# Kernel tuning notes

Measured on AMD Instinct MI355X. Metric: run time of the kernel, lower is better.

Reference implementation:

```python
import jax, jax.numpy as jnp
import numpy as np

V, D, B, P = 50000, 128, 1024, 50
N, E = B * P, B * P
SCALE = 12.0


def _norm(x):
    return jnp.linalg.norm(x, axis=-1, keepdims=True)


def setup_inputs():
    key = jax.random.key(0)
    ks = jax.random.split(key, 32)
    stdv = 1.0 / np.sqrt(D)

    def u(k, shape):
        return jax.random.uniform(k, shape, minval=-stdv, maxval=stdv, dtype=jnp.float32)

    iid = jax.random.randint(ks[0], (N,), 0, V)
    # edges stay inside each session's node block [g*P, (g+1)*P)
    base = jnp.repeat(jnp.arange(B) * P, P)
    edge_src = base + jax.random.randint(ks[1], (E,), 0, P)
    edge_dst = base + jax.random.randint(ks[2], (E,), 0, P)
    node_gid = jnp.repeat(jnp.arange(B), P)          # session id per node
    last_nodes = jnp.arange(B) * P + (P - 1)          # nodes with data['last']==1
    edge_w = jax.random.uniform(ks[3], (E,), minval=0.1, maxval=1.0)
    edge_t = jax.random.uniform(ks[4], (E,))
    params = dict(
        embedding=u(ks[5], (V, D)),
        W1=u(ks[6], (D, 2 * D)), W2=u(ks[7], (D, 2 * D)),
        gru_wih=u(ks[8], (3 * D, 4 * D)), gru_whh=u(ks[9], (3 * D, D)),
        gru_bih=u(ks[10], (3 * D,)), gru_bhh=u(ks[11], (3 * D,)),
        Wxr=u(ks[12], (D, D)), bxr=u(ks[13], (D,)),
        Wxz=u(ks[14], (D, D)), bxz=u(ks[15], (D,)),
        Wxh=u(ks[16], (D, D)), bxh=u(ks[17], (D,)),
        Whr=u(ks[18], (D, D)), bhr=u(ks[19], (D,)),
        Whz=u(ks[20], (D, D)), bhz=u(ks[21], (D,)),
        Whh=u(ks[22], (D, D)), bhh=u(ks[23], (D,)),
        fc_u=u(ks[24], (D, D)),
        fc_vw=u(ks[25], (D, D)), fc_vb=u(ks[26], (D,)),
        fc_e=u(ks[27], (D,)),
        fc_sr=u(ks[28], (2 * D, D)),
    )
    return dict(iid=iid, edge_src=edge_src, edge_dst=edge_dst, node_gid=node_gid,
                last_nodes=last_nodes, edge_w=edge_w, edge_t=edge_t, **params)


def reference(iid, edge_src, edge_dst, node_gid, last_nodes, edge_w, edge_t,
              embedding, W1, W2, gru_wih, gru_whh, gru_bih, gru_bhh,
              Wxr, bxr, Wxz, bxz, Wxh, bxh, Whr, bhr, Whz, bhz, Whh, bhh,
              fc_u, fc_vw, fc_vb, fc_e, fc_sr):
    segN = lambda d, ids: jax.ops.segment_sum(d, ids, num_segments=N)
    feat = embedding[iid]
    feat = feat / (_norm(feat) + 1e-12)

    # --- GGNNLayer (num_layers=1): weighted-mean over in-edges and reversed graph ---
    ws_in = segN(edge_w, edge_dst)
    ws_out = segN(edge_w, edge_src)
    m_in = segN(feat[edge_src] * edge_w[:, None], edge_dst)
    m_out = segN(feat[edge_dst] * edge_w[:, None], edge_src)
    neigh1 = m_in / jnp.where(ws_in > 0, ws_in, 1.0)[:, None]   # zero-degree -> 0 (DGL default)
    neigh2 = m_out / jnp.where(ws_out > 0, ws_out, 1.0)[:, None]
    hn = jnp.concatenate([neigh1 @ W1, neigh2 @ W2], axis=1)    # [N, 4D]
    gi = hn @ gru_wih.T + gru_bih
    gh = feat @ gru_whh.T + gru_bhh
    ir, iz, inn = jnp.split(gi, 3, axis=1)
    hr, hz, hnn = jnp.split(gh, 3, axis=1)
    r = jax.nn.sigmoid(ir + hr)
    z = jax.nn.sigmoid(iz + hz)
    n = jnp.tanh(inn + r * hnn)
    feat = (1.0 - z) * n + z * feat                              # GRUCell update
    feat = feat / jnp.maximum(_norm(feat), 1e-12)                # F.normalize

    # --- GraphGRUODE: one RK4 step on [0, t_end]; per-eval time-filtered symmetric GCN ---
    x = feat
    no_self = edge_src != edge_dst

    def gcn(h, em, W, b):
        # DGL GraphConv norm='both' on the masked graph + its reverse edges
        deg = segN(em, edge_src) + segN(em, edge_dst)
        nrm = jnp.maximum(deg, 1.0) ** -0.5
        hs = h * nrm[:, None]
        me = em[:, None]
        agg = segN(hs[edge_src] * me, edge_dst) + segN(hs[edge_dst] * me, edge_src)
        return (agg * nrm[:, None]) @ W + b

    def f(tv, h):
        em = ((edge_t <= tv) & no_self).astype(h.dtype)
        xr = gcn(x, em, Wxr, bxr)
        xz = gcn(x, em, Wxz, bxz)
        xh = gcn(x, em, Wxh, bxh)
        r_ = jax.nn.sigmoid(xr + gcn(h, em, Whr, bhr))
        z_ = jax.nn.sigmoid(xz + gcn(h, em, Whz, bhz))
        u_ = jnp.tanh(xh + gcn(r_ * h, em, Whh, bhh))
        dh = (1.0 - z_) * (u_ - h)
        return dh / jnp.maximum(_norm(dh), 1e-12)                # F.normalize

    dt = edge_t.max()
    k1 = f(jnp.float32(0.0), feat)
    k2 = f(dt * 0.5, feat + dt * 0.5 * k1)
    k3 = f(dt * 0.5, feat + dt * 0.5 * k2)
    k4 = f(dt, feat + dt * k3)
    feat = feat + (dt / 6.0) * (k1 + 2.0 * k2 + 2.0 * k3 + k4)
    feat = feat / _norm(feat)                                    # torch code divides with no eps here

    # --- AttnReadout (batch_norm disabled, fc_out is None) ---
    fu = feat @ fc_u
    fv = feat[last_nodes] @ fc_vw + fc_vb                        # [B, D]
    e = jax.nn.sigmoid(fu + fv[node_gid]) @ fc_e                 # [N]
    emax = jax.ops.segment_max(e, node_gid, num_segments=B)
    ee = jnp.exp(e - emax[node_gid])
    alpha = ee / jax.ops.segment_sum(ee, node_gid, num_segments=B)[node_gid]
    sr_g = jax.ops.segment_sum(feat * alpha[:, None], node_gid, num_segments=B)
    sr = jnp.concatenate([feat[last_nodes], sr_g], axis=1) @ fc_sr
    sr = sr / (_norm(sr) + 1e-12)

    target = embedding / (_norm(embedding) + 1e-12)
    logits = sr @ target.T                                       # [B, V]
    return jax.nn.log_softmax(SCALE * logits, axis=-1)
```

## Files before the change

### kernel.cpp

```cpp
#include <hip/hip_runtime.h>
#include <math.h>

constexpr int V_ = 50000, D_ = 128, B_ = 1024, P_ = 50;
constexpr int N_ = 51200, E_ = 51200;
constexpr long long NS_ = (long long)N_ * D_;
constexpr float SCALE_ = 12.0f;
constexpr int NBN_L = (V_ + 127) / 128;
constexpr int NBN_P = 392;

typedef unsigned short u16;
typedef __attribute__((ext_vector_type(8))) unsigned short u16x8;
typedef __attribute__((ext_vector_type(8))) __bf16 bf16x8;
typedef __attribute__((ext_vector_type(4))) float f32x4;

static __device__ __forceinline__ float wsum(float v) {
    #pragma unroll
    for (int o = 32; o; o >>= 1) v += __shfl_xor(v, o, 64);
    return v;
}
static __device__ __forceinline__ float wmax(float v) {
    #pragma unroll
    for (int o = 32; o; o >>= 1) v = fmaxf(v, __shfl_xor(v, o, 64));
    return v;
}
static __device__ __forceinline__ float fsig(float x) { return 1.f / (1.f + __expf(-x)); }
static __device__ __forceinline__ float ftanh(float x) { return 2.f / (1.f + __expf(-2.f * x)) - 1.f; }
static __device__ __forceinline__ u16 f2b(float x) {
    unsigned u = __float_as_uint(x);
    u += 0x7fffu + ((u >> 16) & 1u);
    return (u16)(u >> 16);
}
static __device__ __forceinline__ float b2f(u16 u) {
    return __uint_as_float(((unsigned)u) << 16);
}
static __device__ __forceinline__ float redlr(float v) {
    v += __shfl_xor(v, 1, 64); v += __shfl_xor(v, 2, 64);
    v += __shfl_xor(v, 4, 64); v += __shfl_xor(v, 8, 64);
    return v;
}

__global__ void k_embcv(const float* __restrict__ emb, u16* __restrict__ embb,
                        float* __restrict__ rnv) {
    int row = blockIdx.x * 4 + (threadIdx.x >> 6);
    if (row >= V_) return;
    int l = threadIdx.x & 63;
    const float* p = emb + (long long)row * D_;
    float a = p[l], b = p[l + 64];
    float ss = wsum(a * a + b * b);
    if (l == 0) rnv[row] = 1.f / (sqrtf(ss) + 1e-12f);
    u16* q = embb + (long long)row * D_;
    q[l] = f2b(a); q[l + 64] = f2b(b);
}

__global__ void k_dtmax(const float* __restrict__ et, float* __restrict__ dt) {
    __shared__ float s[1024];
    float m = 0.f;
    for (int i = threadIdx.x; i < E_; i += 1024) m = fmaxf(m, et[i]);
    s[threadIdx.x] = m; __syncthreads();
    for (int o = 512; o; o >>= 1) {
        if (threadIdx.x < o) s[threadIdx.x] = fmaxf(s[threadIdx.x], s[threadIdx.x + o]);
        __syncthreads();
    }
    if (threadIdx.x == 0) *dt = s[0];
}

__global__ void k_feat0(const u16* __restrict__ embb, const float* __restrict__ rnv,
                        const int* __restrict__ iid, u16* __restrict__ featb) {
    int row = blockIdx.x * 4 + (threadIdx.x >> 6);
    int l = threadIdx.x & 63;
    int id = iid[row];
    const u16* p = embb + (long long)id * D_;
    float s = rnv[id];
    u16* qb = featb + (long long)row * D_;
    qb[l] = f2b(b2f(p[l]) * s); qb[l + 64] = f2b(b2f(p[l + 64]) * s);
}

__global__ void k_aggA_g(const int* __restrict__ esrc, const int* __restrict__ edst,
                         const float* __restrict__ ew, const u16* __restrict__ featb,
                         u16* __restrict__ m_in, u16* __restrict__ m_out) {
    __shared__ float sfeat[P_ * D_];
    __shared__ float smin[P_ * D_];
    __shared__ float smout[P_ * D_];
    __shared__ int ses[P_], sed[P_];
    __shared__ float sw[P_], swin[P_], swout[P_];
    int g = blockIdx.x, t = threadIdx.x;
    int n0 = g * P_;
    long long base = (long long)n0 * D_;
    for (int i = t; i < P_ * D_; i += 256) {
        sfeat[i] = b2f(featb[base + i]);
        smin[i] = 0.f; smout[i] = 0.f;
    }
    if (t < P_) {
        int E0 = g * P_ + t;
        ses[t] = esrc[E0] - n0;
        sed[t] = edst[E0] - n0;
        sw[t] = ew[E0];
    }
    __syncthreads();
    int d = t & 127;
    for (int e = 0; e < P_; e++) {
        int ls = ses[e], ld = sed[e];
        float w = sw[e];
        if (t < 128) smin[ld * D_ + d] += sfeat[ls * D_ + d] * w;
        else         smout[ls * D_ + d] += sfeat[ld * D_ + d] * w;
    }
    if (t < P_) {
        float wi = 0.f, wo = 0.f;
        for (int e = 0; e < P_; e++) {
            if (sed[e] == t) wi += sw[e];
            if (ses[e] == t) wo += sw[e];
        }
        swin[t] = (wi > 0.f) ? 1.f / wi : 1.f;
        swout[t] = (wo > 0.f) ? 1.f / wo : 1.f;
    }
    __syncthreads();
    for (int i = t; i < P_ * D_; i += 256) {
        int n = i >> 7;
        m_in[base + i] = f2b(smin[i] * swin[n]);
        m_out[base + i] = f2b(smout[i] * swout[n]);
    }
}

__global__ void k_prec_all(const float* __restrict__ W1, const float* __restrict__ W2,
                           const float* __restrict__ wih, const float* __restrict__ whh,
                           const float* __restrict__ bih, const float* __restrict__ bhh,
                           const float* __restrict__ Wxr, const float* __restrict__ Wxz,
                           const float* __restrict__ Whr, const float* __restrict__ Whz,
                           const float* __restrict__ bxr, const float* __restrict__ bxz,
                           const float* __restrict__ bhr, const float* __restrict__ bhz,
                           const float* __restrict__ Wxh, const float* __restrict__ Whh,
                           const float* __restrict__ bxh, const float* __restrict__ bhh2,
                           const float* __restrict__ fcu,
                           u16* __restrict__ BM1t, u16* __restrict__ BM2t, u16* __restrict__ BM3t,
                           u16* __restrict__ Brz1, u16* __restrict__ Brz2,
                           u16* __restrict__ Bu1, u16* __restrict__ Bu2, u16* __restrict__ Bfc,
                           float* __restrict__ b512, float* __restrict__ brz,
                           float* __restrict__ bu) {
    int blk = blockIdx.x, t = threadIdx.x;
    if (blk < 512) {
        const float* W = (blk < 256) ? W1 : W2;
        int coff = (blk < 256) ? 0 : 256;
        u16* Bt = (blk < 256) ? BM1t : BM2t;
        int idx = (blk & 255) * 256 + t;
        int j = idx >> 7, k = idx & 127;
        float s = 0.f;
        if (j < 384) {
            const float* wr = W + (long long)k * 256;
            const float* ir = wih + (long long)j * 512 + coff;
            for (int c = 0; c < 256; c++) s += wr[c] * ir[c];
        }
        Bt[idx] = f2b(s);
    } else if (blk < 768) {
        int idx = (blk - 512) * 256 + t;
        int j = idx >> 7, k = idx & 127;
        float v = 0.f;
        if (j < 256) v = whh[(long long)j * 128 + k];
        else if (j >= 384) v = whh[(long long)(j - 128) * 128 + k];
        BM3t[idx] = f2b(v);
    } else if (blk < 896) {
        int idx = (blk - 768) * 256 + t;
        int c = idx >> 7, k = idx & 127;
        float v1 = (c < 128) ? Wxr[(long long)k * 128 + c] : Wxz[(long long)k * 128 + (c - 128)];
        float v2 = (c < 128) ? Whr[(long long)k * 128 + c] : Whz[(long long)k * 128 + (c - 128)];
        Brz1[idx] = f2b(v1); Brz2[idx] = f2b(v2);
        if (k == 0) brz[c] = (c < 128) ? bxr[c] + bhr[c] : bxz[c - 128] + bhz[c - 128];
    } else if (blk < 960) {
        int idx = (blk - 896) * 256 + t;
        int c = idx >> 7, k = idx & 127;
        Bu1[idx] = f2b(Wxh[(long long)k * 128 + c]);
        Bu2[idx] = f2b(Whh[(long long)k * 128 + c]);
        if (k == 0) bu[c] = bxh[c] + bhh2[c];
    } else if (blk < 1024) {
        int idx = (blk - 960) * 256 + t;
        int c = idx >> 7, k = idx & 127;
        Bfc[idx] = f2b(fcu[(long long)k * 128 + c]);
    } else {
        int j = (blk - 1024) * 256 + t;
        if (j < 512) {
            float v;
            if (j < 256) v = bih[j] + bhh[j];
            else if (j < 384) v = bih[j];
            else v = bhh[j - 128];
            b512[j] = v;
        }
    }
}

template<int NSEG, int ACT>
__launch_bounds__(256)
__global__ void k_mm(const u16* __restrict__ A1, const u16* __restrict__ A2,
                     const u16* __restrict__ A3,
                     const u16* __restrict__ B1, const u16* __restrict__ B2,
                     const u16* __restrict__ B3,
                     const float* __restrict__ bias,
                     u16* __restrict__ C, int ldc, int nbn) {
    __shared__ u16 As[128 * 40];
    __shared__ u16 Bs[128 * 40];
    const int t = threadIdx.x;
    const int bid = blockIdx.x;
    const int xcd = bid & 7, idx = bid >> 3;
    const int nbm8 = gridDim.x / (8 * nbn);
    const int bm = xcd * nbm8 + idx / nbn;
    const int bn = idx % nbn;
    const int lane = t & 63, wid = t >> 6;
    const int wr = wid >> 1, wc = wid & 1;
    const int lr = lane & 15, lh = lane >> 4;
    f32x4 acc[4][4] = {};
    constexpr int KTOT = NSEG * 128;
    for (int ks = 0; ks < KTOT; ks += 32) {
        const u16* Ap = (NSEG == 1) ? A1 : (ks < 128 ? A1 : (ks < 256 ? A2 : A3));
        const u16* Bp = (NSEG == 1) ? B1 : (ks < 128 ? B1 : (ks < 256 ? B2 : B3));
        int kk = ks & 127;
        #pragma unroll
        for (int i = 0; i < 2; i++) {
            int id2 = i * 256 + t;
            int row = id2 >> 2, kl = (id2 & 3) * 8;
            u16x8 va = *(const u16x8*)&Ap[((long long)bm * 128 + row) * 128 + kk + kl];
            *(u16x8*)&As[row * 40 + kl] = va;
            u16x8 vb = *(const u16x8*)&Bp[((long long)bn * 128 + row) * 128 + kk + kl];
            *(u16x8*)&Bs[row * 40 + kl] = vb;
        }
        __syncthreads();
        bf16x8 af[4], bf[4];
        #pragma unroll
        for (int f = 0; f < 4; f++) {
            u16x8 ar = *(const u16x8*)&As[(wr * 64 + f * 16 + lr) * 40 + lh * 8];
            u16x8 br = *(const u16x8*)&Bs[(wc * 64 + f * 16 + lr) * 40 + lh * 8];
            af[f] = __builtin_bit_cast(bf16x8, ar);
            bf[f] = __builtin_bit_cast(bf16x8, br);
        }
        #pragma unroll
        for (int fr = 0; fr < 4; fr++)
            #pragma unroll
            for (int fc = 0; fc < 4; fc++)
                acc[fr][fc] = __builtin_amdgcn_mfma_f32_16x16x32_bf16(af[fr], bf[fc], acc[fr][fc], 0, 0, 0);
        __syncthreads();
    }
    #pragma unroll
    for (int fc = 0; fc < 4; fc++) {
        int col = bn * 128 + wc * 64 + fc * 16 + lr;
        float bb = bias ? bias[col] : 0.f;
        #pragma unroll
        for (int fr = 0; fr < 4; fr++) {
            int rowl = wr * 64 + fr * 16 + lh * 4;
            long long row0 = (long long)bm * 128 + rowl;
            #pragma unroll
            for (int r = 0; r < 4; r++) {
                float v = acc[fr][fc][r] + bb;
                if (ACT == 1) v = fsig(v);
                else if (ACT == 2) v = ftanh(v);
                C[(row0 + r) * (long long)ldc + col] = f2b(v);
            }
        }
    }
}

__global__ void k_gru2(const u16* __restrict__ gih, u16* __restrict__ featb,
                       u16* __restrict__ hb) {
    int row = blockIdx.x * 4 + (threadIdx.x >> 6);
    int l = threadIdx.x & 63;
    const u16* g = gih + (long long)row * 512;
    u16* fb = featb + (long long)row * 128;
    float nv[2]; float ss = 0.f;
    #pragma unroll
    for (int tq = 0; tq < 2; tq++) {
        int d = l + tq * 64;
        float r = fsig(b2f(g[d]));
        float z = fsig(b2f(g[128 + d]));
        float n = ftanh(b2f(g[256 + d]) + r * b2f(g[384 + d]));
        float fv = b2f(fb[d]);
        nv[tq] = (1.f - z) * n + z * fv;
        ss += nv[tq] * nv[tq];
    }
    ss = wsum(ss);
    float s = 1.f / fmaxf(sqrtf(ss), 1e-12f);
    u16 a = f2b(nv[0] * s), b = f2b(nv[1] * s);
    fb[l] = a; fb[l + 64] = b;
    u16* hh = hb + (long long)row * 128;
    hh[l] = a; hh[l + 64] = b;
}

template<int FIN>
__launch_bounds__(512, 8)
__global__ void k_fstep(const int* __restrict__ esrc, const int* __restrict__ edst,
                        const float* __restrict__ et, const float* __restrict__ dtp,
                        float tfac, int h_is_x, int axmode,
                        u16* __restrict__ featb, u16* __restrict__ hb,
                        u16* __restrict__ AXg, u16* __restrict__ RHG, u16* __restrict__ ZG,
                        u16* __restrict__ accg,
                        const u16* __restrict__ Brz1, const u16* __restrict__ Brz2,
                        const float* __restrict__ brz,
                        const u16* __restrict__ Bu1, const u16* __restrict__ Bu2,
                        const float* __restrict__ bu,
                        float accw, float hfac, int first) {
    constexpr int AS = 136;
    __shared__ u16 sAX[64 * AS];
    __shared__ u16 sAH[64 * AS];
    __shared__ float snrm[P_];
    __shared__ int ses[P_], sed[P_], sdeg[P_], soff[P_ + 1], snbr[2 * P_];
    __shared__ float ssqW[4][64];
    const int g = blockIdx.x, t = threadIdx.x;
    const int n0 = g * P_;
    const long long base = (long long)n0 * D_;
    const int wv = t >> 6, lane = t & 63;
    const int lr = lane & 15, lh = lane >> 4;
    const float dt = dtp[0];
    const float tv = tfac * dt;

    for (int i = t; i < 64 * AS; i += 512) { sAX[i] = 0; sAH[i] = 0; }
    if (t < P_) {
        int E0 = g * P_ + t;
        int ss_ = esrc[E0] - n0, dd = edst[E0] - n0;
        bool ml = (ss_ != dd) && (et[E0] <= tv);
        ses[t] = ml ? ss_ : -1;
        sed[t] = ml ? dd : -1;
    }
    __syncthreads();
    if (t < P_) {
        int dg = 0;
        for (int e = 0; e < P_; e++) dg += (ses[e] == t) + (sed[e] == t);
        sdeg[t] = dg;
        snrm[t] = rsqrtf(fmaxf((float)dg, 1.f));
    }
    __syncthreads();
    if (t < 64) {
        int v = (t < P_) ? sdeg[t] : 0;
        int inc = v;
        #pragma unroll
        for (int o = 1; o < 64; o <<= 1) {
            int u = __shfl_up(inc, o, 64);
            if (t >= o) inc += u;
        }
        if (t < P_) soff[t] = inc - v;
        if (t == P_ - 1) soff[P_] = inc;
    }
    __syncthreads();
    if (t < P_) {
        int c = soff[t];
        for (int e = 0; e < P_; e++) {
            if (ses[e] == t) snbr[c++] = sed[e];
            if (sed[e] == t) snbr[c++] = ses[e];
        }
    }
    __syncthreads();

    const int d = t & 127, grp = t >> 7;
    const int nlo = grp * 13, nhi = (grp * 13 + 13 < P_) ? grp * 13 + 13 : P_;
    if (axmode == 2) {
        for (int n = nlo; n < nhi; n++)
            sAX[n * AS + d] = AXg[base + (long long)n * D_ + d];
    } else {
        for (int n = nlo; n < nhi; n++) {
            float a = 0.f;
            for (int j = soff[n]; j < soff[n + 1]; j++) {
                int nb = snbr[j];
                a += b2f(featb[base + (long long)nb * D_ + d]) * snrm[nb];
            }
            u16 v = f2b(a * snrm[n]);
            sAX[n * AS + d] = v;
            if (axmode == 1) AXg[base + (long long)n * D_ + d] = v;
        }
    }
    if (!h_is_x) {
        for (int n = nlo; n < nhi; n++) {
            float a = 0.f;
            for (int j = soff[n]; j < soff[n + 1]; j++) {
                int nb = snbr[j];
                a += b2f(hb[base + (long long)nb * D_ + d]) * snrm[nb];
            }
            sAH[n * AS + d] = f2b(a * snrm[n]);
        }
    }
    __syncthreads();
    {
        const u16* A2 = h_is_x ? sAX : sAH;
        f32x4 acc[4][2] = {};
        for (int ks = 0; ks < 256; ks += 32) {
            const u16* Ap = (ks < 128) ? sAX : A2;
            const u16* Bp = (ks < 128) ? Brz1 : Brz2;
            int kk = ks & 127;
            bf16x8 af[4], bf[2];
            #pragma unroll
            for (int f = 0; f < 4; f++) {
                u16x8 ar = *(const u16x8*)&Ap[(f * 16 + lr) * AS + kk + lh * 8];
                af[f] = __builtin_bit_cast(bf16x8, ar);
            }
            #pragma unroll
            for (int f = 0; f < 2; f++) {
                int col = wv * 32 + f * 16 + lr;
                u16x8 br = *(const u16x8*)&Bp[(long long)col * 128 + kk + lh * 8];
                bf[f] = __builtin_bit_cast(bf16x8, br);
            }
            #pragma unroll
            for (int fr = 0; fr < 4; fr++)
                #pragma unroll
                for (int fc = 0; fc < 2; fc++)
                    acc[fr][fc] = __builtin_amdgcn_mfma_f32_16x16x32_bf16(af[fr], bf[fc], acc[fr][fc], 0, 0, 0);
        }
        #pragma unroll
        for (int fc = 0; fc < 2; fc++) {
            int col = wv * 32 + fc * 16 + lr;
            float bb = brz[col];
            #pragma unroll
            for (int fr = 0; fr < 4; fr++) {
                int row0 = fr * 16 + lh * 4;
                #pragma unroll
                for (int r = 0; r < 4; r++) {
                    int row = row0 + r;
                    if (row < P_) {
                        float v = fsig(acc[fr][fc][r] + bb);
                        long long ix = base + (long long)row * D_;
                        if (col < 128) RHG[ix + col] = f2b(v * b2f(hb[ix + col]));
                        else           ZG[ix + col - 128] = f2b(v);
                    }
                }
            }
        }
    }
    __syncthreads();
    for (int n = nlo; n < nhi; n++) {
        float a = 0.f;
        for (int j = soff[n]; j < soff[n + 1]; j++) {
            int nb = snbr[j];
            a += b2f(RHG[base + (long long)nb * D_ + d]) * snrm[nb];
        }
        sAH[n * AS + d] = f2b(a * snrm[n]);
    }
    __syncthreads();
    const int wr = wv >> 2, wc = wv & 3;
    f32x4 acc[2][2] = {};
    for (int ks = 0; ks < 256; ks += 32) {
        const u16* Ap = (ks < 128) ? sAX : sAH;
        const u16* Bp = (ks < 128) ? Bu1 : Bu2;
        int kk = ks & 127;
        bf16x8 af[2], bf[2];
        #pragma unroll
        for (int f = 0; f < 2; f++) {
            u16x8 ar = *(const u16x8*)&Ap[(wr * 32 + f * 16 + lr) * AS + kk + lh * 8];
            af[f] = __builtin_bit_cast(bf16x8, ar);
        }
        #pragma unroll
        for (int f = 0; f < 2; f++) {
            int col = wc * 32 + f * 16 + lr;
            u16x8 br = *(const u16x8*)&Bp[(long long)col * 128 + kk + lh * 8];
            bf[f] = __builtin_bit_cast(bf16x8, br);
        }
        #pragma unroll
        for (int fr = 0; fr < 2; fr++)
            #pragma unroll
            for (int fc = 0; fc < 2; fc++)
                acc[fr][fc] = __builtin_amdgcn_mfma_f32_16x16x32_bf16(af[fr], bf[fc], acc[fr][fc], 0, 0, 0);
    }
    float pr[2][4] = {};
    #pragma unroll
    for (int fc = 0; fc < 2; fc++) {
        int col = wc * 32 + fc * 16 + lr;
        float bb = bu[col];
        #pragma unroll
        for (int fr = 0; fr < 2; fr++) {
            int row0 = wr * 32 + fr * 16 + lh * 4;
            #pragma unroll
            for (int r = 0; r < 4; r++) {
                int row = row0 + r;
                float v = 0.f;
                if (row < P_) {
                    long long ix = base + (long long)row * D_ + col;
                    float u = ftanh(acc[fr][fc][r] + bb);
                    float z = b2f(ZG[ix]);
                    float hh = b2f(hb[ix]);
                    v = (1.f - z) * (u - hh);
                }
                acc[fr][fc][r] = v;
                pr[fr][r] += v * v;
            }
        }
    }
    #pragma unroll
    for (int fr = 0; fr < 2; fr++)
        #pragma unroll
        for (int r = 0; r < 4; r++) {
            float v = redlr(pr[fr][r]);
            if (lr == 0) ssqW[wc][wr * 32 + fr * 16 + lh * 4 + r] = v;
        }
    __syncthreads();
    if (FIN) {
        float dt6 = dt / 6.f;
        float pr2[2][4] = {};
        #pragma unroll
        for (int fr = 0; fr < 2; fr++) {
            int row0 = wr * 32 + fr * 16 + lh * 4;
            #pragma unroll
            for (int r = 0; r < 4; r++) {
                int row = row0 + r;
                float sc = 0.f;
                if (row < P_) {
                    float ssum = ssqW[0][row] + ssqW[1][row] + ssqW[2][row] + ssqW[3][row];
                    sc = 1.f / fmaxf(sqrtf(ssum), 1e-12f);
                }
                #pragma unroll
                for (int fc = 0; fc < 2; fc++) {
                    int col = wc * 32 + fc * 16 + lr;
                    float fv2 = 0.f;
                    if (row < P_) {
                        long long ix = base + (long long)row * D_ + col;
                        float kv = acc[fr][fc][r] * sc;
                        float an = b2f(accg[ix]) + accw * kv;
                        fv2 = b2f(featb[ix]) + dt6 * an;
                    }
                    acc[fr][fc][r] = fv2;
                    pr2[fr][r] += fv2 * fv2;
                }
            }
        }
        __syncthreads();
        #pragma unroll
        for (int fr = 0; fr < 2; fr++)
            #pragma unroll
            for (int r = 0; r < 4; r++) {
                float v = redlr(pr2[fr][r]);
                if (lr == 0) ssqW[wc][wr * 32 + fr * 16 + lh * 4 + r] = v;
            }
        __syncthreads();
        #pragma unroll
        for (int fr = 0; fr < 2; fr++) {
            int row0 = wr * 32 + fr * 16 + lh * 4;
            #pragma unroll
            for (int r = 0; r < 4; r++) {
                int row = row0 + r;
                if (row >= P_) continue;
                float ssum = ssqW[0][row] + ssqW[1][row] + ssqW[2][row] + ssqW[3][row];
                float s2 = 1.f / sqrtf(ssum);
                #pragma unroll
                for (int fc = 0; fc < 2; fc++) {
                    int col = wc * 32 + fc * 16 + lr;
                    featb[base + (long long)row * D_ + col] = f2b(acc[fr][fc][r] * s2);
                }
            }
        }
    } else {
        #pragma unroll
        for (int fr = 0; fr < 2; fr++) {
            int row0 = wr * 32 + fr * 16 + lh * 4;
            #pragma unroll
            for (int r = 0; r < 4; r++) {
                int row = row0 + r;
                if (row >= P_) continue;
                float ssum = ssqW[0][row] + ssqW[1][row] + ssqW[2][row] + ssqW[3][row];
                float sc = 1.f / fmaxf(sqrtf(ssum), 1e-12f);
                #pragma unroll
                for (int fc = 0; fc < 2; fc++) {
                    int col = wc * 32 + fc * 16 + lr;
                    long long ix = base + (long long)row * D_ + col;
                    float kv = acc[fr][fc][r] * sc;
                    float an = (first ? 0.f : b2f(accg[ix])) + accw * kv;
                    accg[ix] = f2b(an);
                    hb[ix] = f2b(b2f(featb[ix]) + hfac * dt * kv);
                }
            }
        }
    }
}

__launch_bounds__(256)
__global__ void k_readout(const u16* __restrict__ featb, const u16* __restrict__ FU,
                          const int* __restrict__ last,
                          const float* __restrict__ fvw, const float* __restrict__ fvbv,
                          const float* __restrict__ fce, const float* __restrict__ fsr,
                          u16* __restrict__ srb) {
    __shared__ float sfl[128], sfv[128], se[64], sal[64], sin2[256], red[2];
    int g = blockIdx.x, t = threadIdx.x;
    int n0 = g * P_;
    long long ln = last[g];
    if (t < 128) sfl[t] = b2f(featb[ln * 128 + t]);
    __syncthreads();
    if (t < 128) {
        float s = fvbv[t];
        for (int k = 0; k < 128; k++) s += sfl[k] * fvw[(long long)k * 128 + t];
        sfv[t] = s;
        sin2[t] = sfl[t];
    }
    __syncthreads();
    int wid = t >> 6, lane = t & 63;
    float fce0 = fce[lane], fce1 = fce[lane + 64];
    for (int p = wid; p < P_; p += 4) {
        const u16* fu = FU + (long long)(n0 + p) * 128;
        float x0 = b2f(fu[lane]) + sfv[lane];
        float x1 = b2f(fu[lane + 64]) + sfv[lane + 64];
        float s = fsig(x0) * fce0 + fsig(x1) * fce1;
        s = wsum(s);
        if (lane == 0) se[p] = s;
    }
    __syncthreads();
    if (t < 64) {
        float v = (t < P_) ? se[t] : -1e30f;
        float m = wmax(v);
        float ex = (t < P_) ? __expf(v - m) : 0.f;
        float ss = wsum(ex);
        if (t < P_) sal[t] = ex / ss;
    }
    __syncthreads();
    if (t < 128) {
        float s = 0.f;
        for (int p = 0; p < P_; p++)
            s += b2f(featb[(long long)(n0 + p) * 128 + t]) * sal[p];
        sin2[128 + t] = s;
    }
    __syncthreads();
    if (t < 128) {
        float s = 0.f;
        for (int k = 0; k < 256; k++) s += sin2[k] * fsr[(long long)k * 128 + t];
        float ss = wsum(s * s);
        if (lane == 0) red[t >> 6] = ss;
        __syncthreads();
        float nrm = sqrtf(red[0] + red[1]);
        srb[(long long)g * 128 + t] = f2b(s / (nrm + 1e-12f));
    } else {
        __syncthreads();
    }
}

template<int PASS>
__launch_bounds__(256)
__global__ void k_logits(const u16* __restrict__ A, const u16* __restrict__ Bt,
                         const float* __restrict__ rnv, float* __restrict__ rowsumP,
                         const float* __restrict__ logz, float* __restrict__ C) {
    __shared__ u16 As[128 * 40];
    __shared__ u16 Bs[128 * 40];
    __shared__ float sredW[2][128];
    const int t = threadIdx.x;
    const int bid = blockIdx.x;
    const int xcd = bid & 7, idx = bid >> 3;
    const int bm = idx & 7, bnl = idx >> 3;
    const int bn = xcd * 49 + bnl;
    if (bn >= NBN_L) return;
    const int lane = t & 63, wid = t >> 6;
    const int wr = wid >> 1, wc = wid & 1;
    const int lr = lane & 15, lh = lane >> 4;
    f32x4 acc[4][4] = {};
    for (int ks = 0; ks < 128; ks += 32) {
        #pragma unroll
        for (int i = 0; i < 2; i++) {
            int id2 = i * 256 + t;
            int row = id2 >> 2, kl = (id2 & 3) * 8;
            u16x8 va = *(const u16x8*)&A[((long long)bm * 128 + row) * 128 + ks + kl];
            *(u16x8*)&As[row * 40 + kl] = va;
            long long gcol = (long long)bn * 128 + row;
            u16x8 vb;
            if (gcol < V_) vb = *(const u16x8*)&Bt[gcol * 128 + ks + kl];
            else vb = u16x8{0, 0, 0, 0, 0, 0, 0, 0};
            *(u16x8*)&Bs[row * 40 + kl] = vb;
        }
        __syncthreads();
        bf16x8 af[4], bf[4];
        #pragma unroll
        for (int f = 0; f < 4; f++) {
            u16x8 ar = *(const u16x8*)&As[(wr * 64 + f * 16 + lr) * 40 + lh * 8];
            u16x8 br = *(const u16x8*)&Bs[(wc * 64 + f * 16 + lr) * 40 + lh * 8];
            af[f] = __builtin_bit_cast(bf16x8, ar);
            bf[f] = __builtin_bit_cast(bf16x8, br);
        }
        #pragma unroll
        for (int fr = 0; fr < 4; fr++)
            #pragma unroll
            for (int fc = 0; fc < 4; fc++)
                acc[fr][fc] = __builtin_amdgcn_mfma_f32_16x16x32_bf16(af[fr], bf[fc], acc[fr][fc], 0, 0, 0);
        __syncthreads();
    }
    if (PASS == 0) {
        float pr[4][4] = {};
        #pragma unroll
        for (int fc = 0; fc < 4; fc++) {
            int col = bn * 128 + wc * 64 + fc * 16 + lr;
            if (col >= V_) continue;
            float cs = rnv[col] * SCALE_;
            #pragma unroll
            for (int fr = 0; fr < 4; fr++)
                #pragma unroll
                for (int r = 0; r < 4; r++)
                    pr[fr][r] += __expf(acc[fr][fc][r] * cs - SCALE_);
        }
        #pragma unroll
        for (int fr = 0; fr < 4; fr++)
            #pragma unroll
            for (int r = 0; r < 4; r++) {
                float v = redlr(pr[fr][r]);
                if (lr == 0) sredW[wc][wr * 64 + fr * 16 + lh * 4 + r] = v;
            }
        __syncthreads();
        if (t < 128) rowsumP[(long long)(bm * 128 + t) * NBN_P + bn] = sredW[0][t] + sredW[1][t];
    } else {
        if (t < 128) sredW[0][t] = logz[bm * 128 + t];
        __syncthreads();
        #pragma unroll
        for (int fc = 0; fc < 4; fc++) {
            int col = bn * 128 + wc * 64 + fc * 16 + lr;
            if (col >= V_) continue;
            float cs = rnv[col] * SCALE_;
            #pragma unroll
            for (int fr = 0; fr < 4; fr++) {
                int rowl = wr * 64 + fr * 16 + lh * 4;
                long long row0 = (long long)bm * 128 + rowl;
                #pragma unroll
                for (int r = 0; r < 4; r++)
                    C[(row0 + r) * (long long)V_ + col] = acc[fr][fc][r] * cs - SCALE_ - sredW[0][rowl + r];
            }
        }
    }
}

__global__ void k_rsum(const float* __restrict__ rowsumP, float* __restrict__ logz) {
    int t = threadIdx.x;
    int row = blockIdx.x * 128 + (t >> 1);
    int half = t & 1;
    const float* p = rowsumP + (long long)row * NBN_P;
    float s = 0.f;
    int j0 = half ? 196 : 0, j1 = half ? NBN_L : 196;
    for (int j = j0; j < j1; j++) s += p[j];
    s += __shfl_xor(s, 1);
    if (!half) logz[row] = logf(s);
}

extern "C" void kernel_launch(void* const* d_in, const int* in_sizes, int n_in,
                              void* d_out, int out_size, void* d_ws, size_t ws_size,
                              hipStream_t stream) {
    const int* iid   = (const int*)d_in[0];
    const int* esrc  = (const int*)d_in[1];
    const int* edst  = (const int*)d_in[2];
    const int* last  = (const int*)d_in[4];
    const float* ew  = (const float*)d_in[5];
    const float* et  = (const float*)d_in[6];
    const float* emb = (const float*)d_in[7];
    const float* W1  = (const float*)d_in[8];
    const float* W2  = (const float*)d_in[9];
    const float* wih = (const float*)d_in[10];
    const float* whh = (const float*)d_in[11];
    const float* bih = (const float*)d_in[12];
    const float* bhh = (const float*)d_in[13];
    const float* Wxr = (const float*)d_in[14]; const float* bxr = (const float*)d_in[15];
    const float* Wxz = (const float*)d_in[16]; const float* bxz = (const float*)d_in[17];
    const float* Wxh = (const float*)d_in[18]; const float* bxh = (const float*)d_in[19];
    const float* Whr = (const float*)d_in[20]; const float* bhr = (const float*)d_in[21];
    const float* Whz = (const float*)d_in[22]; const float* bhz = (const float*)d_in[23];
    const float* Whh = (const float*)d_in[24]; const float* bhh2 = (const float*)d_in[25];
    const float* fcu = (const float*)d_in[26];
    const float* fvw = (const float*)d_in[27]; const float* fvbv = (const float*)d_in[28];
    const float* fce = (const float*)d_in[29];
    const float* fsr = (const float*)d_in[30];
    float* out = (float*)d_out;

    char* w = (char*)d_ws;
    auto alloc = [&](size_t bytes) { char* p = w; w += (bytes + 255) & ~(size_t)255; return p; };
    u16* ACCb    = (u16*)alloc(NS_ * 2);
    u16* FEATb   = (u16*)alloc(NS_ * 2);
    u16* Hb      = (u16*)alloc(NS_ * 2);
    u16* MINb    = (u16*)alloc(NS_ * 2);
    u16* MOUTb   = (u16*)alloc(NS_ * 2);
    u16* GIHb    = (u16*)alloc(NS_ * 8);
    u16* AXb     = GIHb;
    u16* RHG     = GIHb + NS_;
    u16* ZG      = GIHb + 2 * NS_;
    u16* FUb     = MINb;
    u16* embb    = (u16*)alloc((long long)V_ * 128 * 2);
    u16* srb     = (u16*)alloc(B_ * 128 * 2);
    u16* BM1t    = (u16*)alloc(512 * 128 * 2);
    u16* BM2t    = (u16*)alloc(512 * 128 * 2);
    u16* BM3t    = (u16*)alloc(512 * 128 * 2);
    u16* Brz1    = (u16*)alloc(256 * 128 * 2);
    u16* Brz2    = (u16*)alloc(256 * 128 * 2);
    u16* Bu1     = (u16*)alloc(128 * 128 * 2);
    u16* Bu2     = (u16*)alloc(128 * 128 * 2);
    u16* Bfc     = (u16*)alloc(128 * 128 * 2);
    float* b512  = (float*)alloc(512 * 4);
    float* brz   = (float*)alloc(256 * 4);
    float* bu    = (float*)alloc(128 * 4);
    float* dtp   = (float*)alloc(64 * 4);
    float* rnv   = (float*)alloc((long long)V_ * 4);
    float* rowsumP = (float*)alloc((long long)B_ * NBN_P * 4);
    float* logz  = (float*)alloc(B_ * 4);

    k_embcv<<<(V_ + 3) / 4, 256, 0, stream>>>(emb, embb, rnv);
    k_dtmax<<<1, 1024, 0, stream>>>(et, dtp);
    k_feat0<<<N_ / 4, 256, 0, stream>>>(embb, rnv, iid, FEATb);

    k_aggA_g<<<B_, 256, 0, stream>>>(esrc, edst, ew, FEATb, MINb, MOUTb);
    k_prec_all<<<1026, 256, 0, stream>>>(W1, W2, wih, whh, bih, bhh,
                                         Wxr, Wxz, Whr, Whz, bxr, bxz, bhr, bhz,
                                         Wxh, Whh, bxh, bhh2, fcu,
                                         BM1t, BM2t, BM3t, Brz1, Brz2, Bu1, Bu2, Bfc,
                                         b512, brz, bu);
    k_mm<3, 0><<<1600, 256, 0, stream>>>(MINb, MOUTb, FEATb, BM1t, BM2t, BM3t, b512, GIHb, 512, 4);
    k_gru2<<<N_ / 4, 256, 0, stream>>>(GIHb, FEATb, Hb);

    k_fstep<0><<<B_, 512, 0, stream>>>(esrc, edst, et, dtp, 0.0f, 1, 0, FEATb, Hb, AXb, RHG, ZG,
                                       ACCb, Brz1, Brz2, brz, Bu1, Bu2, bu, 1.f, 0.5f, 1);
    k_fstep<0><<<B_, 512, 0, stream>>>(esrc, edst, et, dtp, 0.5f, 0, 1, FEATb, Hb, AXb, RHG, ZG,
                                       ACCb, Brz1, Brz2, brz, Bu1, Bu2, bu, 2.f, 0.5f, 0);
    k_fstep<0><<<B_, 512, 0, stream>>>(esrc, edst, et, dtp, 0.5f, 0, 2, FEATb, Hb, AXb, RHG, ZG,
                                       ACCb, Brz1, Brz2, brz, Bu1, Bu2, bu, 2.f, 1.0f, 0);
    k_fstep<1><<<B_, 512, 0, stream>>>(esrc, edst, et, dtp, 1.0f, 0, 0, FEATb, Hb, AXb, RHG, ZG,
                                       ACCb, Brz1, Brz2, brz, Bu1, Bu2, bu, 1.f, 0.0f, 0);

    k_mm<1, 0><<<400, 256, 0, stream>>>(FEATb, nullptr, nullptr, Bfc, nullptr, nullptr,
                                        nullptr, FUb, 128, 1);
    k_readout<<<B_, 256, 0, stream>>>(FEATb, FUb, last, fvw, fvbv, fce, fsr, srb);

    k_logits<0><<<3136, 256, 0, stream>>>(srb, embb, rnv, rowsumP, nullptr, nullptr);
    k_rsum<<<8, 256, 0, stream>>>(rowsumP, logz);
    k_logits<1><<<3136, 256, 0, stream>>>(srb, embb, rnv, nullptr, logz, out);
}
```

Before: 681.3 us.

## Fuse RK4 stages two and three into one kernel, reuse graph and AX in shared memory

The two middle RK4 stages share the same time threshold, so they now run in one kernel. The second pass skips rebuilding the edge lists and the AX aggregation and reuses them from shared memory, which removes the global AX round trip and one launch. Kernel parameters become template constants, and the shared-memory zeroing now covers only the padding rows. The risk is correctness: the second pass reads hb written by other threads within the same block, so it depends on the intervening barrier, but this holds because each session is local to its block.

```diff
diff --git a/kernel.cpp b/kernel.cpp
--- a/kernel.cpp
+++ b/kernel.cpp
@@ -280,88 +280,76 @@
     hh[l] = a; hh[l + 64] = b;
 }
 
-template<int FIN>
-__launch_bounds__(512, 8)
-__global__ void k_fstep(const int* __restrict__ esrc, const int* __restrict__ edst,
-                        const float* __restrict__ et, const float* __restrict__ dtp,
-                        float tfac, int h_is_x, int axmode,
-                        u16* __restrict__ featb, u16* __restrict__ hb,
-                        u16* __restrict__ AXg, u16* __restrict__ RHG, u16* __restrict__ ZG,
-                        u16* __restrict__ accg,
-                        const u16* __restrict__ Brz1, const u16* __restrict__ Brz2,
-                        const float* __restrict__ brz,
-                        const u16* __restrict__ Bu1, const u16* __restrict__ Bu2,
-                        const float* __restrict__ bu,
-                        float accw, float hfac, int first) {
+template<int FIN, int H_IS_X, int SKIP, int FIRST>
+static __device__ __forceinline__ void fstep_body(
+    const int* __restrict__ esrc, const int* __restrict__ edst,
+    const float* __restrict__ et,
+    float tfac, float dt, float accw, float hfac,
+    u16* __restrict__ featb, u16* __restrict__ hb,
+    u16* __restrict__ RHG, u16* __restrict__ ZG, u16* __restrict__ accg,
+    const u16* __restrict__ Brz1, const u16* __restrict__ Brz2,
+    const float* __restrict__ brz,
+    const u16* __restrict__ Bu1, const u16* __restrict__ Bu2,
+    const float* __restrict__ bu,
+    u16* sAX, u16* sAH, float* snrm,
+    int* ses, int* sed, int* sdeg, int* soff, int* snbr,
+    float (*ssqW)[64]) {
     constexpr int AS = 136;
-    __shared__ u16 sAX[64 * AS];
-    __shared__ u16 sAH[64 * AS];
-    __shared__ float snrm[P_];
-    __shared__ int ses[P_], sed[P_], sdeg[P_], soff[P_ + 1], snbr[2 * P_];
-    __shared__ float ssqW[4][64];
     const int g = blockIdx.x, t = threadIdx.x;
     const int n0 = g * P_;
     const long long base = (long long)n0 * D_;
     const int wv = t >> 6, lane = t & 63;
     const int lr = lane & 15, lh = lane >> 4;
-    const float dt = dtp[0];
     const float tv = tfac * dt;
-
-    for (int i = t; i < 64 * AS; i += 512) { sAX[i] = 0; sAH[i] = 0; }
-    if (t < P_) {
-        int E0 = g * P_ + t;
-        int ss_ = esrc[E0] - n0, dd = edst[E0] - n0;
-        bool ml = (ss_ != dd) && (et[E0] <= tv);
-        ses[t] = ml ? ss_ : -1;
-        sed[t] = ml ? dd : -1;
-    }
-    __syncthreads();
-    if (t < P_) {
-        int dg = 0;
-        for (int e = 0; e < P_; e++) dg += (ses[e] == t) + (sed[e] == t);
-        sdeg[t] = dg;
-        snrm[t] = rsqrtf(fmaxf((float)dg, 1.f));
-    }
-    __syncthreads();
-    if (t < 64) {
-        int v = (t < P_) ? sdeg[t] : 0;
-        int inc = v;
-        #pragma unroll
-        for (int o = 1; o < 64; o <<= 1) {
-            int u = __shfl_up(inc, o, 64);
-            if (t >= o) inc += u;
-        }
-        if (t < P_) soff[t] = inc - v;
-        if (t == P_ - 1) soff[P_] = inc;
-    }
-    __syncthreads();
-    if (t < P_) {
-        int c = soff[t];
-        for (int e = 0; e < P_; e++) {
-            if (ses[e] == t) snbr[c++] = sed[e];
-            if (sed[e] == t) snbr[c++] = ses[e];
-        }
-    }
-    __syncthreads();
-
     const int d = t & 127, grp = t >> 7;
     const int nlo = grp * 13, nhi = (grp * 13 + 13 < P_) ? grp * 13 + 13 : P_;
-    if (axmode == 2) {
-        for (int n = nlo; n < nhi; n++)
-            sAX[n * AS + d] = AXg[base + (long long)n * D_ + d];
-    } else {
+
+    if (!SKIP) {
+        if (t < P_) {
+            int E0 = g * P_ + t;
+            int ss_ = esrc[E0] - n0, dd = edst[E0] - n0;
+            bool ml = (ss_ != dd) && (et[E0] <= tv);
+            ses[t] = ml ? ss_ : -1;
+            sed[t] = ml ? dd : -1;
+        }
+        __syncthreads();
+        if (t < P_) {
+            int dg = 0;
+            for (int e = 0; e < P_; e++) dg += (ses[e] == t) + (sed[e] == t);
+            sdeg[t] = dg;
+            snrm[t] = rsqrtf(fmaxf((float)dg, 1.f));
+        }
+        __syncthreads();
+        if (t < 64) {
+            int v = (t < P_) ? sdeg[t] : 0;
+            int inc = v;
+            #pragma unroll
+            for (int o = 1; o < 64; o <<= 1) {
+                int u = __shfl_up(inc, o, 64);
+                if (t >= o) inc += u;
+            }
+            if (t < P_) soff[t] = inc - v;
+            if (t == P_ - 1) soff[P_] = inc;
+        }
+        __syncthreads();
+        if (t < P_) {
+            int c = soff[t];
+            for (int e = 0; e < P_; e++) {
+                if (ses[e] == t) snbr[c++] = sed[e];
+                if (sed[e] == t) snbr[c++] = ses[e];
+            }
+        }
+        __syncthreads();
         for (int n = nlo; n < nhi; n++) {
             float a = 0.f;
             for (int j = soff[n]; j < soff[n + 1]; j++) {
                 int nb = snbr[j];
                 a += b2f(featb[base + (long long)nb * D_ + d]) * snrm[nb];
             }
-            u16 v = f2b(a * snrm[n]);
-            sAX[n * AS + d] = v;
-            if (axmode == 1) AXg[base + (long long)n * D_ + d] = v;
-        }
-    }
-    if (!h_is_x) {
+            sAX[n * AS + d] = f2b(a * snrm[n]);
+        }
+    }
+    if (!H_IS_X) {
         for (int n = nlo; n < nhi; n++) {
             float a = 0.f;
             for (int j = soff[n]; j < soff[n + 1]; j++) {
@@ -373,7 +361,7 @@
     }
     __syncthreads();
     {
-        const u16* A2 = h_is_x ? sAX : sAH;
+        const u16* A2 = H_IS_X ? sAX : sAH;
         f32x4 acc[4][2] = {};
         for (int ks = 0; ks < 256; ks += 32) {
             const u16* Ap = (ks < 128) ? sAX : A2;
@@ -552,13 +540,73 @@
                     int col = wc * 32 + fc * 16 + lr;
                     long long ix = base + (long long)row * D_ + col;
                     float kv = acc[fr][fc][r] * sc;
-                    float an = (first ? 0.f : b2f(accg[ix])) + accw * kv;
+                    float an = (FIRST ? 0.f : b2f(accg[ix])) + accw * kv;
                     accg[ix] = f2b(an);
                     hb[ix] = f2b(b2f(featb[ix]) + hfac * dt * kv);
                 }
             }
         }
     }
+}
+
+#define FSTEP_SHARED_DECL                                              \
+    __shared__ u16 sAX[64 * 136];                                      \
+    __shared__ u16 sAH[64 * 136];                                      \
+    __shared__ float snrm[P_];                                         \
+    __shared__ int ses[P_], sed[P_], sdeg[P_], soff[P_ + 1], snbr[2 * P_]; \
+    __shared__ float ssqW[4][64];                                      \
+    for (int i = P_ * 136 + threadIdx.x; i < 64 * 136; i += 512) { sAX[i] = 0; sAH[i] = 0; }
+
+__launch_bounds__(512, 8)
+__global__ void k_fstepA(const int* __restrict__ esrc, const int* __restrict__ edst,
+                         const float* __restrict__ et, const float* __restrict__ dtp,
+                         u16* __restrict__ featb, u16* __restrict__ hb,
+                         u16* __restrict__ RHG, u16* __restrict__ ZG, u16* __restrict__ accg,
+                         const u16* __restrict__ Brz1, const u16* __restrict__ Brz2,
+                         const float* __restrict__ brz,
+                         const u16* __restrict__ Bu1, const u16* __restrict__ Bu2,
+                         const float* __restrict__ bu) {
+    FSTEP_SHARED_DECL
+    const float dt = dtp[0];
+    fstep_body<0, 1, 0, 1>(esrc, edst, et, 0.0f, dt, 1.f, 0.5f,
+                           featb, hb, RHG, ZG, accg, Brz1, Brz2, brz, Bu1, Bu2, bu,
+                           sAX, sAH, snrm, ses, sed, sdeg, soff, snbr, ssqW);
+}
+
+__launch_bounds__(512, 8)
+__global__ void k_fstepBC(const int* __restrict__ esrc, const int* __restrict__ edst,
+                          const float* __restrict__ et, const float* __restrict__ dtp,
+                          u16* __restrict__ featb, u16* __restrict__ hb,
+                          u16* __restrict__ RHG, u16* __restrict__ ZG, u16* __restrict__ accg,
+                          const u16* __restrict__ Brz1, const u16* __restrict__ Brz2,
+                          const float* __restrict__ brz,
+                          const u16* __restrict__ Bu1, const u16* __restrict__ Bu2,
+                          const float* __restrict__ bu) {
+    FSTEP_SHARED_DECL
+    const float dt = dtp[0];
+    fstep_body<0, 0, 0, 0>(esrc, edst, et, 0.5f, dt, 2.f, 0.5f,
+                           featb, hb, RHG, ZG, accg, Brz1, Brz2, brz, Bu1, Bu2, bu,
+                           sAX, sAH, snrm, ses, sed, sdeg, soff, snbr, ssqW);
+    __syncthreads();
+    fstep_body<0, 0, 1, 0>(esrc, edst, et, 0.5f, dt, 2.f, 1.0f,
+                           featb, hb, RHG, ZG, accg, Brz1, Brz2, brz, Bu1, Bu2, bu,
+                           sAX, sAH, snrm, ses, sed, sdeg, soff, snbr, ssqW);
+}
+
+__launch_bounds__(512, 8)
+__global__ void k_fstepD(const int* __restrict__ esrc, const int* __restrict__ edst,
+                         const float* __restrict__ et, const float* __restrict__ dtp,
+                         u16* __restrict__ featb, u16* __restrict__ hb,
+                         u16* __restrict__ RHG, u16* __restrict__ ZG, u16* __restrict__ accg,
+                         const u16* __restrict__ Brz1, const u16* __restrict__ Brz2,
+                         const float* __restrict__ brz,
+                         const u16* __restrict__ Bu1, const u16* __restrict__ Bu2,
+                         const float* __restrict__ bu) {
+    FSTEP_SHARED_DECL
+    const float dt = dtp[0];
+    fstep_body<1, 0, 0, 0>(esrc, edst, et, 1.0f, dt, 1.f, 0.0f,
+                           featb, hb, RHG, ZG, accg, Brz1, Brz2, brz, Bu1, Bu2, bu,
+                           sAX, sAH, snrm, ses, sed, sdeg, soff, snbr, ssqW);
 }
 
 __launch_bounds__(256)
@@ -756,7 +804,6 @@
     u16* MINb    = (u16*)alloc(NS_ * 2);
     u16* MOUTb   = (u16*)alloc(NS_ * 2);
     u16* GIHb    = (u16*)alloc(NS_ * 8);
-    u16* AXb     = GIHb;
     u16* RHG     = GIHb + NS_;
     u16* ZG      = GIHb + 2 * NS_;
     u16* FUb     = MINb;
@@ -791,14 +838,12 @@
     k_mm<3, 0><<<1600, 256, 0, stream>>>(MINb, MOUTb, FEATb, BM1t, BM2t, BM3t, b512, GIHb, 512, 4);
     k_gru2<<<N_ / 4, 256, 0, stream>>>(GIHb, FEATb, Hb);
 
-    k_fstep<0><<<B_, 512, 0, stream>>>(esrc, edst, et, dtp, 0.0f, 1, 0, FEATb, Hb, AXb, RHG, ZG,
-                                       ACCb, Brz1, Brz2, brz, Bu1, Bu2, bu, 1.f, 0.5f, 1);
-    k_fstep<0><<<B_, 512, 0, stream>>>(esrc, edst, et, dtp, 0.5f, 0, 1, FEATb, Hb, AXb, RHG, ZG,
-                                       ACCb, Brz1, Brz2, brz, Bu1, Bu2, bu, 2.f, 0.5f, 0);
-    k_fstep<0><<<B_, 512, 0, stream>>>(esrc, edst, et, dtp, 0.5f, 0, 2, FEATb, Hb, AXb, RHG, ZG,
-                                       ACCb, Brz1, Brz2, brz, Bu1, Bu2, bu, 2.f, 1.0f, 0);
-    k_fstep<1><<<B_, 512, 0, stream>>>(esrc, edst, et, dtp, 1.0f, 0, 0, FEATb, Hb, AXb, RHG, ZG,
-                                       ACCb, Brz1, Brz2, brz, Bu1, Bu2, bu, 1.f, 0.0f, 0);
+    k_fstepA<<<B_, 512, 0, stream>>>(esrc, edst, et, dtp, FEATb, Hb, RHG, ZG, ACCb,
+                                     Brz1, Brz2, brz, Bu1, Bu2, bu);
+    k_fstepBC<<<B_, 512, 0, stream>>>(esrc, edst, et, dtp, FEATb, Hb, RHG, ZG, ACCb,
+                                      Brz1, Brz2, brz, Bu1, Bu2, bu);
+    k_fstepD<<<B_, 512, 0, stream>>>(esrc, edst, et, dtp, FEATb, Hb, RHG, ZG, ACCb,
+                                     Brz1, Brz2, brz, Bu1, Bu2, bu);
 
     k_mm<1, 0><<<400, 256, 0, stream>>>(FEATb, nullptr, nullptr, Bfc, nullptr, nullptr,
                                         nullptr, FUb, 128, 1);
```

New measurement: 969.6 us. 1.42x slower.
